# Kernel optimization log

Hardware: AMD Instinct MI355X
Metric: run time of the kernel (lower is better)

## Reference

```python
import jax, jax.numpy as jnp
import numpy as np

B, N, IN_DIM, HID, OUT, HEADS = 2, 1024, 64, 64, 64, 4
PHD1, PHD2 = HID // HEADS, OUT // HEADS
SLOPE = 0.2  # PyG GATv2Conv default negative_slope
EPS = 1e-12  # F.normalize eps


def _gatv2_dense(x, Wl, Wr, att, bias, heads, phd, mask):
    """Dense GATv2 layer over a full adjacency mask.
    x: [B,N,Din]; Wl/Wr: [Din, heads*phd]; att: [heads,phd]; bias: [heads*phd];
    mask: [N,N] bool, mask[i,j]=True means edge j->i exists.
    """
    Bb, Nn, _ = x.shape
    xl = (x @ Wl).reshape(Bb, Nn, heads, phd)  # source features
    xr = (x @ Wr).reshape(Bb, Nn, heads, phd)  # target features
    # s[b,i,j,h,p] = leaky_relu(xr[b,i] + xl[b,j])  (GATv2)
    s = jax.nn.leaky_relu(xr[:, :, None] + xl[:, None, :], SLOPE)
    e = jnp.einsum('bijhp,hp->bijh', s, att)  # [B,Ni,Nj,H]
    e = jnp.where(mask[None, :, :, None], e, -jnp.inf)
    alpha = jax.nn.softmax(e, axis=2)  # softmax over source nodes j
    out = jnp.einsum('bijh,bjhp->bihp', alpha, xl).reshape(Bb, Nn, heads * phd)
    return out + bias


def setup_inputs() -> dict:
    key = jax.random.key(0)
    ks = jax.random.split(key, 10)
    sc = 0.1
    return {
        'x': jax.random.normal(ks[0], (B, N, IN_DIM), jnp.float32),
        'embedding': jax.random.normal(ks[1], (N, HID), jnp.float32),
        'Wl1': jax.random.normal(ks[2], (IN_DIM, HEADS * PHD1), jnp.float32) * sc,
        'Wr1': jax.random.normal(ks[3], (IN_DIM, HEADS * PHD1), jnp.float32) * sc,
        'att1': jax.random.normal(ks[4], (HEADS, PHD1), jnp.float32) * sc,
        'b1': jnp.zeros((HEADS * PHD1,), jnp.float32),
        'Wl2': jax.random.normal(ks[5], (HID, HEADS * PHD2), jnp.float32) * sc,
        'Wr2': jax.random.normal(ks[6], (HID, HEADS * PHD2), jnp.float32) * sc,
        'att2': jax.random.normal(ks[7], (HEADS, PHD2), jnp.float32) * sc,
        'b2': jnp.zeros((HEADS * PHD2,), jnp.float32),
    }


def reference(x, embedding, Wl1, Wr1, att1, b1, Wl2, Wr2, att2, b2):
    # AdaptiveAdjacency: cosine-similarity adjacency; only its nonzero pattern is used.
    norm = jnp.maximum(jnp.linalg.norm(embedding, axis=1, keepdims=True), EPS)
    ne = embedding / norm
    adj = ne @ ne.T  # [N,N]
    # edge set = adj.nonzero(); GATv2Conv(add_self_loops=True) guarantees diagonal
    mask = (adj != 0) | jnp.eye(N, dtype=bool)
    h = jax.nn.relu(_gatv2_dense(x, Wl1, Wr1, att1, b1, HEADS, PHD1, mask))
    # dropout(0.3) in eval mode -> identity
    return _gatv2_dense(h, Wl2, Wr2, att2, b2, HEADS, PHD2, mask)
```

## Files before the change

### kernel.cpp

```cpp
#include <hip/hip_runtime.h>
#include <math.h>

#define NN 1024
#define BB 2
#define D 64
#define NHEAD 4
#define LOG2E 1.4426950408889634f
#define MST 65

template <int CTRL>
__device__ __forceinline__ float dpp_mov(float x) {
    int xi = __builtin_bit_cast(int, x);
    int r = __builtin_amdgcn_update_dpp(0, xi, CTRL, 0xF, 0xF, true);
    return __builtin_bit_cast(float, r);
}
template <int CTRL>
__device__ __forceinline__ unsigned dpp_movi(unsigned x) {
    int r = __builtin_amdgcn_update_dpp(0, (int)x, CTRL, 0xF, 0xF, true);
    return (unsigned)r;
}

__device__ __forceinline__ float dpp_rowsum16(float t) {
    t += dpp_mov<0x111>(t);
    t += dpp_mov<0x112>(t);
    t += dpp_mov<0x114>(t);
    t += dpp_mov<0x118>(t);
    return t;
}

__global__ __launch_bounds__(256) void k_mask_gemm(
    const float* __restrict__ emb, unsigned char* __restrict__ mask,
    const float* __restrict__ A, const float* __restrict__ Wl,
    const float* __restrict__ Wr, const float* __restrict__ att,
    float* __restrict__ xl, float* __restrict__ xr, float* __restrict__ alE)
{
    __shared__ float SH[64 * MST * 2];
    int tid = threadIdx.x;
    if (blockIdx.x < 256) {
        float* As = SH;
        float* Bs = SH + 64 * MST;
        int ib = (blockIdx.x & 15) << 6;
        int jb = (blockIdx.x >> 4) << 6;

        #pragma unroll
        for (int r = 0; r < 4; ++r) {
            int q = tid + (r << 8);
            int row = q >> 4, c4 = (q & 15) << 2;
            float4 a = *(const float4*)&emb[(ib + row) * D + c4];
            float4 b = *(const float4*)&emb[(jb + row) * D + c4];
            As[row * MST + c4 + 0] = a.x; As[row * MST + c4 + 1] = a.y;
            As[row * MST + c4 + 2] = a.z; As[row * MST + c4 + 3] = a.w;
            Bs[row * MST + c4 + 0] = b.x; Bs[row * MST + c4 + 1] = b.y;
            Bs[row * MST + c4 + 2] = b.z; Bs[row * MST + c4 + 3] = b.w;
        }
        __syncthreads();

        int i0 = (tid >> 4) << 2;
        int j0 = (tid & 15) << 2;
        float acc[4][4] = {};
        #pragma unroll 8
        for (int k = 0; k < 64; ++k) {
            float a0 = As[(i0 + 0) * MST + k];
            float a1 = As[(i0 + 1) * MST + k];
            float a2 = As[(i0 + 2) * MST + k];
            float a3 = As[(i0 + 3) * MST + k];
            float b0 = Bs[(j0 + 0) * MST + k];
            float b1 = Bs[(j0 + 1) * MST + k];
            float b2 = Bs[(j0 + 2) * MST + k];
            float b3 = Bs[(j0 + 3) * MST + k];
            acc[0][0] = fmaf(a0, b0, acc[0][0]); acc[0][1] = fmaf(a0, b1, acc[0][1]);
            acc[0][2] = fmaf(a0, b2, acc[0][2]); acc[0][3] = fmaf(a0, b3, acc[0][3]);
            acc[1][0] = fmaf(a1, b0, acc[1][0]); acc[1][1] = fmaf(a1, b1, acc[1][1]);
            acc[1][2] = fmaf(a1, b2, acc[1][2]); acc[1][3] = fmaf(a1, b3, acc[1][3]);
            acc[2][0] = fmaf(a2, b0, acc[2][0]); acc[2][1] = fmaf(a2, b1, acc[2][1]);
            acc[2][2] = fmaf(a2, b2, acc[2][2]); acc[2][3] = fmaf(a2, b3, acc[2][3]);
            acc[3][0] = fmaf(a3, b0, acc[3][0]); acc[3][1] = fmaf(a3, b1, acc[3][1]);
            acc[3][2] = fmaf(a3, b2, acc[3][2]); acc[3][3] = fmaf(a3, b3, acc[3][3]);
        }
        #pragma unroll
        for (int r = 0; r < 4; ++r) {
            int gi = ib + i0 + r;
            uchar4 m;
            m.x = (acc[r][0] != 0.f || gi == jb + j0 + 0) ? 1 : 0;
            m.y = (acc[r][1] != 0.f || gi == jb + j0 + 1) ? 1 : 0;
            m.z = (acc[r][2] != 0.f || gi == jb + j0 + 2) ? 1 : 0;
            m.w = (acc[r][3] != 0.f || gi == jb + j0 + 3) ? 1 : 0;
            *(uchar4*)&mask[gi * NN + jb + j0] = m;
        }
    } else {
        float* wl = SH;
        float* wr = SH + 4096;
        for (int t = tid; t < 4096; t += 256) { wl[t] = Wl[t]; wr[t] = Wr[t]; }
        __syncthreads();
        int r = (blockIdx.x - 256) * 4 + (tid >> 6);
        int c = tid & 63;
        float av = att[c];
        const float* arow = A + r * 64;
        float accl = 0.f, accr = 0.f;
        #pragma unroll
        for (int p = 0; p < 64; ++p) {
            float a = arow[p];
            accl = fmaf(a, wl[p * 64 + c], accl);
            accr = fmaf(a, wr[p * 64 + c], accr);
        }
        int cp = (((c >> 2) & 3) << 4) | ((c >> 4) << 2) | (c & 3);
        xl[r * 64 + cp] = accl;
        xr[r * 64 + c] = accr;
        float t = dpp_rowsum16(accl * av);
        if ((c & 15) == 15) alE[(r << 2) | (c >> 4)] = 0.6f * LOG2E * t;
    }
}

template <bool RELU, bool FUSEG>
__global__ __launch_bounds__(256, 2) void k_attn(
    const float* __restrict__ xlp, const float* __restrict__ xr,
    const float* __restrict__ att, const float* __restrict__ alE,
    const float* __restrict__ bias, const unsigned char* __restrict__ mask,
    float* __restrict__ out,
    const float* __restrict__ Wl2, const float* __restrict__ Wr2,
    const float* __restrict__ att2,
    float* __restrict__ xl2, float* __restrict__ xr2, float* __restrict__ alE2)
{
    __shared__ __align__(16) float XS[8192];
    __shared__ float Opart[4][4][4][64];
    __shared__ float Lpart[4][4][4][NHEAD];
    __shared__ float RES[4][64];

    int tid = threadIdx.x;
    int wave = tid >> 6, lane = tid & 63;
    int h = lane & 3, jl = lane >> 2;
    int b = blockIdx.x >> 8;
    int i0 = (blockIdx.x & 255) << 2;

    const float* xlb = xlp + (b << 16);

    float at[16], xr0f[16], xr1f[16], xr2f[16], xr3f[16];
    {
        const float* ap = att + (h << 4);
        const float* r0 = xr + (((b << 10) + i0) << 6) + (h << 4);
        const float* r1 = r0 + 64;
        const float* r2 = r0 + 128;
        const float* r3 = r0 + 192;
        #pragma unroll
        for (int c = 0; c < 4; ++c) {
            *(float4*)&at[c << 2]   = *(const float4*)(ap + (c << 2));
            *(float4*)&xr0f[c << 2] = *(const float4*)(r0 + (c << 2));
            *(float4*)&xr1f[c << 2] = *(const float4*)(r1 + (c << 2));
            *(float4*)&xr2f[c << 2] = *(const float4*)(r2 + (c << 2));
            *(float4*)&xr3f[c << 2] = *(const float4*)(r3 + (c << 2));
        }
        #pragma unroll
        for (int p = 0; p < 16; ++p) at[p] *= 0.4f * LOG2E;
    }
    float ar0, ar1, ar2, ar3;
    {
        float s0[4], s1[4], s2[4], s3[4];
        #pragma unroll
        for (int c = 0; c < 4; ++c) {
            float t0 = 0.f, t1 = 0.f, t2 = 0.f, t3 = 0.f;
            #pragma unroll
            for (int r = 0; r < 4; ++r) {
                int p = (c << 2) + r;
                float a = at[p];
                t0 = fmaf(a, xr0f[p], t0);
                t1 = fmaf(a, xr1f[p], t1);
                t2 = fmaf(a, xr2f[p], t2);
                t3 = fmaf(a, xr3f[p], t3);
            }
            s0[c] = t0; s1[c] = t1; s2[c] = t2; s3[c] = t3;
        }
        ar0 = 1.5f * ((s0[0] + s0[1]) + (s0[2] + s0[3]));
        ar1 = 1.5f * ((s1[0] + s1[1]) + (s1[2] + s1[3]));
        ar2 = 1.5f * ((s2[0] + s2[1]) + (s2[2] + s2[3]));
        ar3 = 1.5f * ((s3[0] + s3[1]) + (s3[2] + s3[3]));
    }

    unsigned mb0, mb1, mb2, mb3;
    {
        const unsigned char* mp = mask + i0 * NN + (wave << 8) + jl;
        int hh = h << 6;
        unsigned n0 = (unsigned)mp[hh] | ((unsigned)mp[hh + 16] << 1)
                    | ((unsigned)mp[hh + 32] << 2) | ((unsigned)mp[hh + 48] << 3);
        mp += NN;
        unsigned n1 = (unsigned)mp[hh] | ((unsigned)mp[hh + 16] << 1)
                    | ((unsigned)mp[hh + 32] << 2) | ((unsigned)mp[hh + 48] << 3);
        mp += NN;
        unsigned n2 = (unsigned)mp[hh] | ((unsigned)mp[hh + 16] << 1)
                    | ((unsigned)mp[hh + 32] << 2) | ((unsigned)mp[hh + 48] << 3);
        mp += NN;
        unsigned n3 = (unsigned)mp[hh] | ((unsigned)mp[hh + 16] << 1)
                    | ((unsigned)mp[hh + 32] << 2) | ((unsigned)mp[hh + 48] << 3);
        unsigned v0 = n0 << (h << 2), v1 = n1 << (h << 2);
        unsigned v2 = n2 << (h << 2), v3 = n3 << (h << 2);
        v0 |= dpp_movi<0xB1>(v0); v0 |= dpp_movi<0x4E>(v0);
        v1 |= dpp_movi<0xB1>(v1); v1 |= dpp_movi<0x4E>(v1);
        v2 |= dpp_movi<0xB1>(v2); v2 |= dpp_movi<0x4E>(v2);
        v3 |= dpp_movi<0xB1>(v3); v3 |= dpp_movi<0x4E>(v3);
        mb0 = v0; mb1 = v1; mb2 = v2; mb3 = v3;
    }

    float O0[16], O1[16], O2[16], O3[16];
    float lq0 = 0.f, lq1 = 0.f, lq2 = 0.f, lq3 = 0.f;
    #pragma unroll
    for (int p = 0; p < 16; ++p) { O0[p] = 0.f; O1[p] = 0.f; O2[p] = 0.f; O3[p] = 0.f; }

    const float* tb = xlb + (wave << 14);
    float* XB = XS + (wave << 11);
    int l4 = lane << 2;
    int rowoff = (lane >> 4) << 6;
    int sb = (lane & 15) ^ (lane >> 4);
    int A0 = rowoff + (sb << 2);
    int A1 = rowoff + ((sb ^ 4) << 2);
    int qx = (jl >> 2) & 1;
    int rb = (jl << 6) + ((h ^ (jl & 3)) << 2);
    const float* alp = alE + (b << 12) + (wave << 10) + lane;

    float4 gA0, gA1, gA2, gA3, gB0, gB1, gB2, gB3;
    {
        const float* p = tb + l4;
        gA0 = *(const float4*)p;         gA1 = *(const float4*)(p + 256);
        gA2 = *(const float4*)(p + 512); gA3 = *(const float4*)(p + 768);
        p = tb + 1024 + l4;
        gB0 = *(const float4*)p;         gB1 = *(const float4*)(p + 256);
        gB2 = *(const float4*)(p + 512); gB3 = *(const float4*)(p + 768);
        *(float4*)&XB[A0] = gA0;         *(float4*)&XB[256 + A1] = gA1;
        *(float4*)&XB[512 + A0] = gA2;   *(float4*)&XB[768 + A1] = gA3;
        p = tb + 2048 + l4;
        gA0 = *(const float4*)p;         gA1 = *(const float4*)(p + 256);
        gA2 = *(const float4*)(p + 512); gA3 = *(const float4*)(p + 768);
    }

    #pragma unroll 2
    for (int s = 0; s < 16; ++s) {
        if ((s & 1) == 0) {
            if (s < 15) {
                float* w = XB + (((s + 1) & 1) << 10);
                *(float4*)&w[A0] = gB0;         *(float4*)&w[256 + A1] = gB1;
                *(float4*)&w[512 + A0] = gB2;   *(float4*)&w[768 + A1] = gB3;
            }
            if (s < 13) {
                const float* p = tb + ((s + 3) << 10) + l4;
                gB0 = *(const float4*)p;         gB1 = *(const float4*)(p + 256);
                gB2 = *(const float4*)(p + 512); gB3 = *(const float4*)(p + 768);
            }
        } else {
            if (s < 15) {
                float* w = XB + (((s + 1) & 1) << 10);
                *(float4*)&w[A0] = gA0;         *(float4*)&w[256 + A1] = gA1;
                *(float4*)&w[512 + A0] = gA2;   *(float4*)&w[768 + A1] = gA3;
            }
            if (s < 13) {
                const float* p = tb + ((s + 3) << 10) + l4;
                gA0 = *(const float4*)p;         gA1 = *(const float4*)(p + 256);
                gA2 = *(const float4*)(p + 512); gA3 = *(const float4*)(p + 768);
            }
        }

        const float* XBr = XB + ((s & 1) << 10);
        float xv[16];
        *(float4*)&xv[0]  = *(const float4*)&XBr[rb + (((0 ^ qx)) << 4)];
        *(float4*)&xv[4]  = *(const float4*)&XBr[rb + (((1 ^ qx)) << 4)];
        *(float4*)&xv[8]  = *(const float4*)&XBr[rb + (((2 ^ qx)) << 4)];
        *(float4*)&xv[12] = *(const float4*)&XBr[rb + (((3 ^ qx)) << 4)];
        float alr = alp[s << 6];
        bool m0 = (mb0 >> s) & 1, m1 = (mb1 >> s) & 1;
        bool m2 = (mb2 >> s) & 1, m3 = (mb3 >> s) & 1;

        float s0[4], s1[4], s2[4], s3[4];
        #pragma unroll
        for (int c = 0; c < 4; ++c) {
            float t0 = 0.f, t1 = 0.f, t2 = 0.f, t3 = 0.f;
            #pragma unroll
            for (int r = 0; r < 4; ++r) {
                int p = (c << 2) + r;
                float a = at[p], xvv = xv[p];
                t0 = fmaf(a, __builtin_fabsf(xr0f[p] + xvv), t0);
                t1 = fmaf(a, __builtin_fabsf(xr1f[p] + xvv), t1);
                t2 = fmaf(a, __builtin_fabsf(xr2f[p] + xvv), t2);
                t3 = fmaf(a, __builtin_fabsf(xr3f[p] + xvv), t3);
            }
            s0[c] = t0; s1[c] = t1; s2[c] = t2; s3[c] = t3;
        }
        float e0 = ((s0[0] + s0[1]) + (s0[2] + s0[3])) + (ar0 + alr);
        float e1 = ((s1[0] + s1[1]) + (s1[2] + s1[3])) + (ar1 + alr);
        float e2 = ((s2[0] + s2[1]) + (s2[2] + s2[3])) + (ar2 + alr);
        float e3 = ((s3[0] + s3[1]) + (s3[2] + s3[3])) + (ar3 + alr);
        float pe0 = m0 ? __builtin_amdgcn_exp2f(e0) : 0.f;
        float pe1 = m1 ? __builtin_amdgcn_exp2f(e1) : 0.f;
        float pe2 = m2 ? __builtin_amdgcn_exp2f(e2) : 0.f;
        float pe3 = m3 ? __builtin_amdgcn_exp2f(e3) : 0.f;
        lq0 += pe0; lq1 += pe1; lq2 += pe2; lq3 += pe3;
        #pragma unroll
        for (int p = 0; p < 16; ++p) {
            float xvv = xv[p];
            O0[p] = fmaf(pe0, xvv, O0[p]);
            O1[p] = fmaf(pe1, xvv, O1[p]);
            O2[p] = fmaf(pe2, xvv, O2[p]);
            O3[p] = fmaf(pe3, xvv, O3[p]);
        }
    }

    if constexpr (FUSEG) {
        __syncthreads();
        for (int t = tid; t < 4096; t += 256) { XS[t] = Wl2[t]; XS[4096 + t] = Wr2[t]; }
    }

    #pragma unroll
    for (int p = 0; p < 16; ++p) {
        O0[p] += dpp_mov<0x114>(O0[p]);  O0[p] += dpp_mov<0x118>(O0[p]);
        O1[p] += dpp_mov<0x114>(O1[p]);  O1[p] += dpp_mov<0x118>(O1[p]);
        O2[p] += dpp_mov<0x114>(O2[p]);  O2[p] += dpp_mov<0x118>(O2[p]);
        O3[p] += dpp_mov<0x114>(O3[p]);  O3[p] += dpp_mov<0x118>(O3[p]);
    }
    lq0 += dpp_mov<0x114>(lq0);  lq0 += dpp_mov<0x118>(lq0);
    lq1 += dpp_mov<0x114>(lq1);  lq1 += dpp_mov<0x118>(lq1);
    lq2 += dpp_mov<0x114>(lq2);  lq2 += dpp_mov<0x118>(lq2);
    lq3 += dpp_mov<0x114>(lq3);  lq3 += dpp_mov<0x118>(lq3);

    if ((lane & 15) >= 12) {
        int k = lane >> 4;
        #pragma unroll
        for (int c = 0; c < 4; ++c) {
            *(float4*)&Opart[0][wave][k][(h << 4) + (c << 2)] = *(const float4*)&O0[c << 2];
            *(float4*)&Opart[1][wave][k][(h << 4) + (c << 2)] = *(const float4*)&O1[c << 2];
            *(float4*)&Opart[2][wave][k][(h << 4) + (c << 2)] = *(const float4*)&O2[c << 2];
            *(float4*)&Opart[3][wave][k][(h << 4) + (c << 2)] = *(const float4*)&O3[c << 2];
        }
        Lpart[0][wave][k][h] = lq0;
        Lpart[1][wave][k][h] = lq1;
        Lpart[2][wave][k][h] = lq2;
        Lpart[3][wave][k][h] = lq3;
    }
    __syncthreads();

    {
        int ii = tid >> 6, c = tid & 63;
        float o = 0.f, l = 0.f;
        #pragma unroll
        for (int w = 0; w < 4; ++w)
            #pragma unroll
            for (int k = 0; k < 4; ++k) {
                o += Opart[ii][w][k][c];
                l += Lpart[ii][w][k][c >> 4];
            }
        float res = o / l + bias[c];
        if (RELU) res = fmaxf(res, 0.f);
        if constexpr (FUSEG) {
            RES[ii][c] = res;
        } else {
            out[((b << 10) + i0 + ii) * D + c] = res;
        }
    }

    if constexpr (FUSEG) {
        __syncthreads();
        int ii = tid >> 6, c = tid & 63;
        int rr = (blockIdx.x << 2) + ii;
        float av = att2[c];
        const float* arow = &RES[ii][0];
        float accl = 0.f, accr = 0.f;
        #pragma unroll
        for (int p = 0; p < 64; ++p) {
            float a = arow[p];
            accl = fmaf(a, XS[p * 64 + c], accl);
            accr = fmaf(a, XS[4096 + p * 64 + c], accr);
        }
        int cp = (((c >> 2) & 3) << 4) | ((c >> 4) << 2) | (c & 3);
        xl2[rr * 64 + cp] = accl;
        xr2[rr * 64 + c] = accr;
        float t = dpp_rowsum16(accl * av);
        if ((c & 15) == 15) alE2[(rr << 2) | (c >> 4)] = 0.6f * LOG2E * t;
    }
}

extern "C" void kernel_launch(void* const* d_in, const int* in_sizes, int n_in,
                              void* d_out, int out_size, void* d_ws, size_t ws_size,
                              hipStream_t stream) {
    const float* x    = (const float*)d_in[0];
    const float* emb  = (const float*)d_in[1];
    const float* Wl1  = (const float*)d_in[2];
    const float* Wr1  = (const float*)d_in[3];
    const float* att1 = (const float*)d_in[4];
    const float* b1   = (const float*)d_in[5];
    const float* Wl2  = (const float*)d_in[6];
    const float* Wr2  = (const float*)d_in[7];
    const float* att2 = (const float*)d_in[8];
    const float* b2   = (const float*)d_in[9];
    float* out = (float*)d_out;

    unsigned char* mask = (unsigned char*)d_ws;
    float* xl   = (float*)(mask + NN * NN);
    float* xr   = xl + BB * NN * D;
    float* xl2  = xr + BB * NN * D;
    float* alE  = xl2 + BB * NN * D;
    float* xr2  = alE + BB * NN * NHEAD;
    float* alE2 = xr2 + BB * NN * D;

    k_mask_gemm<<<256 + BB * NN / 4, 256, 0, stream>>>(emb, mask, x, Wl1, Wr1, att1, xl, xr, alE);

    k_attn<true, true><<<BB * NN / 4, 256, 0, stream>>>(
        xl, xr, att1, alE, b1, mask, xl2 ,
        Wl2, Wr2, att2, xl2, xr2, alE2);

    k_attn<false, false><<<BB * NN / 4, 256, 0, stream>>>(
        xl2, xr2, att2, alE2, b2, mask, out,
        Wl2, Wr2, att2, xl2, xr2, alE2 );
}
```

Baseline: 122.0 us.

## Process eight target rows per attention block instead of four

Each attention block now handles 8 target nodes instead of 4, so every source-feature tile staged in shared memory is reused across twice as many rows, halving global xl traffic per output. Grid size is halved to 256 blocks and launch bounds drop to one block per CU to fit the doubled register accumulators. This trades occupancy and parallelism (only 256 blocks on a 256-CU part) for reuse, and raises register pressure with risk of spills.

```diff
diff --git a/kernel.cpp b/kernel.cpp
--- a/kernel.cpp
+++ b/kernel.cpp
@@ -112,7 +112,7 @@
 }
 
 template <bool RELU, bool FUSEG>
-__global__ __launch_bounds__(256, 2) void k_attn(
+__global__ __launch_bounds__(256, 1) void k_attn(
     const float* __restrict__ xlp, const float* __restrict__ xr,
     const float* __restrict__ att, const float* __restrict__ alE,
     const float* __restrict__ bias, const unsigned char* __restrict__ mask,
@@ -122,42 +122,46 @@
     float* __restrict__ xl2, float* __restrict__ xr2, float* __restrict__ alE2)
 {
     __shared__ __align__(16) float XS[8192];
-    __shared__ float Opart[4][4][4][64];
-    __shared__ float Lpart[4][4][4][NHEAD];
-    __shared__ float RES[4][64];
+    __shared__ float Opart[8][4][4][64];
+    __shared__ float Lpart[8][4][4][NHEAD];
+    __shared__ float RES[8][64];
 
     int tid = threadIdx.x;
     int wave = tid >> 6, lane = tid & 63;
     int h = lane & 3, jl = lane >> 2;
-    int b = blockIdx.x >> 8;
-    int i0 = (blockIdx.x & 255) << 2;
+    int b = blockIdx.x >> 7;
+    int i0 = (blockIdx.x & 127) << 3;
 
     const float* xlb = xlp + (b << 16);
 
-    float at[16], xr0f[16], xr1f[16], xr2f[16], xr3f[16];
+    float at[16];
+    float xr0f[16], xr1f[16], xr2f[16], xr3f[16];
+    float xr4f[16], xr5f[16], xr6f[16], xr7f[16];
     {
         const float* ap = att + (h << 4);
         const float* r0 = xr + (((b << 10) + i0) << 6) + (h << 4);
-        const float* r1 = r0 + 64;
-        const float* r2 = r0 + 128;
-        const float* r3 = r0 + 192;
         #pragma unroll
         for (int c = 0; c < 4; ++c) {
             *(float4*)&at[c << 2]   = *(const float4*)(ap + (c << 2));
             *(float4*)&xr0f[c << 2] = *(const float4*)(r0 + (c << 2));
-            *(float4*)&xr1f[c << 2] = *(const float4*)(r1 + (c << 2));
-            *(float4*)&xr2f[c << 2] = *(const float4*)(r2 + (c << 2));
-            *(float4*)&xr3f[c << 2] = *(const float4*)(r3 + (c << 2));
+            *(float4*)&xr1f[c << 2] = *(const float4*)(r0 + 64 + (c << 2));
+            *(float4*)&xr2f[c << 2] = *(const float4*)(r0 + 128 + (c << 2));
+            *(float4*)&xr3f[c << 2] = *(const float4*)(r0 + 192 + (c << 2));
+            *(float4*)&xr4f[c << 2] = *(const float4*)(r0 + 256 + (c << 2));
+            *(float4*)&xr5f[c << 2] = *(const float4*)(r0 + 320 + (c << 2));
+            *(float4*)&xr6f[c << 2] = *(const float4*)(r0 + 384 + (c << 2));
+            *(float4*)&xr7f[c << 2] = *(const float4*)(r0 + 448 + (c << 2));
         }
         #pragma unroll
         for (int p = 0; p < 16; ++p) at[p] *= 0.4f * LOG2E;
     }
-    float ar0, ar1, ar2, ar3;
+    float ar0, ar1, ar2, ar3, ar4, ar5, ar6, ar7;
     {
-        float s0[4], s1[4], s2[4], s3[4];
+        float s0[4], s1[4], s2[4], s3[4], s4[4], s5[4], s6[4], s7[4];
         #pragma unroll
         for (int c = 0; c < 4; ++c) {
             float t0 = 0.f, t1 = 0.f, t2 = 0.f, t3 = 0.f;
+            float t4 = 0.f, t5 = 0.f, t6 = 0.f, t7 = 0.f;
             #pragma unroll
             for (int r = 0; r < 4; ++r) {
                 int p = (c << 2) + r;
@@ -166,43 +170,58 @@
                 t1 = fmaf(a, xr1f[p], t1);
                 t2 = fmaf(a, xr2f[p], t2);
                 t3 = fmaf(a, xr3f[p], t3);
+                t4 = fmaf(a, xr4f[p], t4);
+                t5 = fmaf(a, xr5f[p], t5);
+                t6 = fmaf(a, xr6f[p], t6);
+                t7 = fmaf(a, xr7f[p], t7);
             }
             s0[c] = t0; s1[c] = t1; s2[c] = t2; s3[c] = t3;
+            s4[c] = t4; s5[c] = t5; s6[c] = t6; s7[c] = t7;
         }
         ar0 = 1.5f * ((s0[0] + s0[1]) + (s0[2] + s0[3]));
         ar1 = 1.5f * ((s1[0] + s1[1]) + (s1[2] + s1[3]));
         ar2 = 1.5f * ((s2[0] + s2[1]) + (s2[2] + s2[3]));
         ar3 = 1.5f * ((s3[0] + s3[1]) + (s3[2] + s3[3]));
-    }
-
-    unsigned mb0, mb1, mb2, mb3;
+        ar4 = 1.5f * ((s4[0] + s4[1]) + (s4[2] + s4[3]));
+        ar5 = 1.5f * ((s5[0] + s5[1]) + (s5[2] + s5[3]));
+        ar6 = 1.5f * ((s6[0] + s6[1]) + (s6[2] + s6[3]));
+        ar7 = 1.5f * ((s7[0] + s7[1]) + (s7[2] + s7[3]));
+    }
+
+    unsigned mb0, mb1, mb2, mb3, mb4, mb5, mb6, mb7;
     {
         const unsigned char* mp = mask + i0 * NN + (wave << 8) + jl;
         int hh = h << 6;
-        unsigned n0 = (unsigned)mp[hh] | ((unsigned)mp[hh + 16] << 1)
-                    | ((unsigned)mp[hh + 32] << 2) | ((unsigned)mp[hh + 48] << 3);
-        mp += NN;
-        unsigned n1 = (unsigned)mp[hh] | ((unsigned)mp[hh + 16] << 1)
-                    | ((unsigned)mp[hh + 32] << 2) | ((unsigned)mp[hh + 48] << 3);
-        mp += NN;
-        unsigned n2 = (unsigned)mp[hh] | ((unsigned)mp[hh + 16] << 1)
-                    | ((unsigned)mp[hh + 32] << 2) | ((unsigned)mp[hh + 48] << 3);
-        mp += NN;
-        unsigned n3 = (unsigned)mp[hh] | ((unsigned)mp[hh + 16] << 1)
-                    | ((unsigned)mp[hh + 32] << 2) | ((unsigned)mp[hh + 48] << 3);
-        unsigned v0 = n0 << (h << 2), v1 = n1 << (h << 2);
-        unsigned v2 = n2 << (h << 2), v3 = n3 << (h << 2);
+        unsigned nv[8];
+        #pragma unroll
+        for (int rw = 0; rw < 8; ++rw) {
+            nv[rw] = (unsigned)mp[hh] | ((unsigned)mp[hh + 16] << 1)
+                   | ((unsigned)mp[hh + 32] << 2) | ((unsigned)mp[hh + 48] << 3);
+            mp += NN;
+        }
+        unsigned sh = h << 2;
+        unsigned v0 = nv[0] << sh, v1 = nv[1] << sh, v2 = nv[2] << sh, v3 = nv[3] << sh;
+        unsigned v4 = nv[4] << sh, v5 = nv[5] << sh, v6 = nv[6] << sh, v7 = nv[7] << sh;
         v0 |= dpp_movi<0xB1>(v0); v0 |= dpp_movi<0x4E>(v0);
         v1 |= dpp_movi<0xB1>(v1); v1 |= dpp_movi<0x4E>(v1);
         v2 |= dpp_movi<0xB1>(v2); v2 |= dpp_movi<0x4E>(v2);
         v3 |= dpp_movi<0xB1>(v3); v3 |= dpp_movi<0x4E>(v3);
+        v4 |= dpp_movi<0xB1>(v4); v4 |= dpp_movi<0x4E>(v4);
+        v5 |= dpp_movi<0xB1>(v5); v5 |= dpp_movi<0x4E>(v5);
+        v6 |= dpp_movi<0xB1>(v6); v6 |= dpp_movi<0x4E>(v6);
+        v7 |= dpp_movi<0xB1>(v7); v7 |= dpp_movi<0x4E>(v7);
         mb0 = v0; mb1 = v1; mb2 = v2; mb3 = v3;
-    }
-
-    float O0[16], O1[16], O2[16], O3[16];
+        mb4 = v4; mb5 = v5; mb6 = v6; mb7 = v7;
+    }
+
+    float O0[16], O1[16], O2[16], O3[16], O4[16], O5[16], O6[16], O7[16];
     float lq0 = 0.f, lq1 = 0.f, lq2 = 0.f, lq3 = 0.f;
+    float lq4 = 0.f, lq5 = 0.f, lq6 = 0.f, lq7 = 0.f;
     #pragma unroll
-    for (int p = 0; p < 16; ++p) { O0[p] = 0.f; O1[p] = 0.f; O2[p] = 0.f; O3[p] = 0.f; }
+    for (int p = 0; p < 16; ++p) {
+        O0[p] = 0.f; O1[p] = 0.f; O2[p] = 0.f; O3[p] = 0.f;
+        O4[p] = 0.f; O5[p] = 0.f; O6[p] = 0.f; O7[p] = 0.f;
+    }
 
     const float* tb = xlb + (wave << 14);
     float* XB = XS + (wave << 11);
@@ -265,11 +284,14 @@
         float alr = alp[s << 6];
         bool m0 = (mb0 >> s) & 1, m1 = (mb1 >> s) & 1;
         bool m2 = (mb2 >> s) & 1, m3 = (mb3 >> s) & 1;
-
-        float s0[4], s1[4], s2[4], s3[4];
+        bool m4 = (mb4 >> s) & 1, m5 = (mb5 >> s) & 1;
+        bool m6 = (mb6 >> s) & 1, m7 = (mb7 >> s) & 1;
+
+        float s0[4], s1[4], s2[4], s3[4], s4[4], s5[4], s6[4], s7[4];
         #pragma unroll
         for (int c = 0; c < 4; ++c) {
             float t0 = 0.f, t1 = 0.f, t2 = 0.f, t3 = 0.f;
+            float t4 = 0.f, t5 = 0.f, t6 = 0.f, t7 = 0.f;
             #pragma unroll
             for (int r = 0; r < 4; ++r) {
                 int p = (c << 2) + r;
@@ -278,18 +300,32 @@
                 t1 = fmaf(a, __builtin_fabsf(xr1f[p] + xvv), t1);
                 t2 = fmaf(a, __builtin_fabsf(xr2f[p] + xvv), t2);
                 t3 = fmaf(a, __builtin_fabsf(xr3f[p] + xvv), t3);
+                t4 = fmaf(a, __builtin_fabsf(xr4f[p] + xvv), t4);
+                t5 = fmaf(a, __builtin_fabsf(xr5f[p] + xvv), t5);
+                t6 = fmaf(a, __builtin_fabsf(xr6f[p] + xvv), t6);
+                t7 = fmaf(a, __builtin_fabsf(xr7f[p] + xvv), t7);
             }
             s0[c] = t0; s1[c] = t1; s2[c] = t2; s3[c] = t3;
+            s4[c] = t4; s5[c] = t5; s6[c] = t6; s7[c] = t7;
         }
         float e0 = ((s0[0] + s0[1]) + (s0[2] + s0[3])) + (ar0 + alr);
         float e1 = ((s1[0] + s1[1]) + (s1[2] + s1[3])) + (ar1 + alr);
         float e2 = ((s2[0] + s2[1]) + (s2[2] + s2[3])) + (ar2 + alr);
         float e3 = ((s3[0] + s3[1]) + (s3[2] + s3[3])) + (ar3 + alr);
+        float e4 = ((s4[0] + s4[1]) + (s4[2] + s4[3])) + (ar4 + alr);
+        float e5 = ((s5[0] + s5[1]) + (s5[2] + s5[3])) + (ar5 + alr);
+        float e6 = ((s6[0] + s6[1]) + (s6[2] + s6[3])) + (ar6 + alr);
+        float e7 = ((s7[0] + s7[1]) + (s7[2] + s7[3])) + (ar7 + alr);
         float pe0 = m0 ? __builtin_amdgcn_exp2f(e0) : 0.f;
         float pe1 = m1 ? __builtin_amdgcn_exp2f(e1) : 0.f;
         float pe2 = m2 ? __builtin_amdgcn_exp2f(e2) : 0.f;
         float pe3 = m3 ? __builtin_amdgcn_exp2f(e3) : 0.f;
+        float pe4 = m4 ? __builtin_amdgcn_exp2f(e4) : 0.f;
+        float pe5 = m5 ? __builtin_amdgcn_exp2f(e5) : 0.f;
+        float pe6 = m6 ? __builtin_amdgcn_exp2f(e6) : 0.f;
+        float pe7 = m7 ? __builtin_amdgcn_exp2f(e7) : 0.f;
         lq0 += pe0; lq1 += pe1; lq2 += pe2; lq3 += pe3;
+        lq4 += pe4; lq5 += pe5; lq6 += pe6; lq7 += pe7;
         #pragma unroll
         for (int p = 0; p < 16; ++p) {
             float xvv = xv[p];
@@ -297,6 +333,10 @@
             O1[p] = fmaf(pe1, xvv, O1[p]);
             O2[p] = fmaf(pe2, xvv, O2[p]);
             O3[p] = fmaf(pe3, xvv, O3[p]);
+            O4[p] = fmaf(pe4, xvv, O4[p]);
+            O5[p] = fmaf(pe5, xvv, O5[p]);
+            O6[p] = fmaf(pe6, xvv, O6[p]);
+            O7[p] = fmaf(pe7, xvv, O7[p]);
         }
     }
 
@@ -311,11 +351,19 @@
         O1[p] += dpp_mov<0x114>(O1[p]);  O1[p] += dpp_mov<0x118>(O1[p]);
         O2[p] += dpp_mov<0x114>(O2[p]);  O2[p] += dpp_mov<0x118>(O2[p]);
         O3[p] += dpp_mov<0x114>(O3[p]);  O3[p] += dpp_mov<0x118>(O3[p]);
+        O4[p] += dpp_mov<0x114>(O4[p]);  O4[p] += dpp_mov<0x118>(O4[p]);
+        O5[p] += dpp_mov<0x114>(O5[p]);  O5[p] += dpp_mov<0x118>(O5[p]);
+        O6[p] += dpp_mov<0x114>(O6[p]);  O6[p] += dpp_mov<0x118>(O6[p]);
+        O7[p] += dpp_mov<0x114>(O7[p]);  O7[p] += dpp_mov<0x118>(O7[p]);
     }
     lq0 += dpp_mov<0x114>(lq0);  lq0 += dpp_mov<0x118>(lq0);
     lq1 += dpp_mov<0x114>(lq1);  lq1 += dpp_mov<0x118>(lq1);
     lq2 += dpp_mov<0x114>(lq2);  lq2 += dpp_mov<0x118>(lq2);
     lq3 += dpp_mov<0x114>(lq3);  lq3 += dpp_mov<0x118>(lq3);
+    lq4 += dpp_mov<0x114>(lq4);  lq4 += dpp_mov<0x118>(lq4);
+    lq5 += dpp_mov<0x114>(lq5);  lq5 += dpp_mov<0x118>(lq5);
+    lq6 += dpp_mov<0x114>(lq6);  lq6 += dpp_mov<0x118>(lq6);
+    lq7 += dpp_mov<0x114>(lq7);  lq7 += dpp_mov<0x118>(lq7);
 
     if ((lane & 15) >= 12) {
         int k = lane >> 4;
@@ -325,51 +373,67 @@
             *(float4*)&Opart[1][wave][k][(h << 4) + (c << 2)] = *(const float4*)&O1[c << 2];
             *(float4*)&Opart[2][wave][k][(h << 4) + (c << 2)] = *(const float4*)&O2[c << 2];
             *(float4*)&Opart[3][wave][k][(h << 4) + (c << 2)] = *(const float4*)&O3[c << 2];
+            *(float4*)&Opart[4][wave][k][(h << 4) + (c << 2)] = *(const float4*)&O4[c << 2];
+            *(float4*)&Opart[5][wave][k][(h << 4) + (c << 2)] = *(const float4*)&O5[c << 2];
+            *(float4*)&Opart[6][wave][k][(h << 4) + (c << 2)] = *(const float4*)&O6[c << 2];
+            *(float4*)&Opart[7][wave][k][(h << 4) + (c << 2)] = *(const float4*)&O7[c << 2];
         }
         Lpart[0][wave][k][h] = lq0;
         Lpart[1][wave][k][h] = lq1;
         Lpart[2][wave][k][h] = lq2;
         Lpart[3][wave][k][h] = lq3;
+        Lpart[4][wave][k][h] = lq4;
+        Lpart[5][wave][k][h] = lq5;
+        Lpart[6][wave][k][h] = lq6;
+        Lpart[7][wave][k][h] = lq7;
     }
     __syncthreads();
 
     {
-        int ii = tid >> 6, c = tid & 63;
-        float o = 0.f, l = 0.f;
-        #pragma unroll
-        for (int w = 0; w < 4; ++w)
+        int c = tid & 63;
+        #pragma unroll
+        for (int pass = 0; pass < 2; ++pass) {
+            int ii = (tid >> 6) + (pass << 2);
+            float o = 0.f, l = 0.f;
             #pragma unroll
-            for (int k = 0; k < 4; ++k) {
-                o += Opart[ii][w][k][c];
-                l += Lpart[ii][w][k][c >> 4];
-            }
-        float res = o / l + bias[c];
-        if (RELU) res = fmaxf(res, 0.f);
-        if constexpr (FUSEG) {
-            RES[ii][c] = res;
-        } else {
-            out[((b << 10) + i0 + ii) * D + c] = res;
+            for (int w = 0; w < 4; ++w)
+                #pragma unroll
+                for (int k = 0; k < 4; ++k) {
+                    o += Opart[ii][w][k][c];
+                    l += Lpart[ii][w][k][c >> 4];
+                }
+            float res = o / l + bias[c];
+            if (RELU) res = fmaxf(res, 0.f);
+            if constexpr (FUSEG) {
+                RES[ii][c] = res;
+            } else {
+                out[((b << 10) + i0 + ii) * D + c] = res;
+            }
         }
     }
 
     if constexpr (FUSEG) {
         __syncthreads();
-        int ii = tid >> 6, c = tid & 63;
-        int rr = (blockIdx.x << 2) + ii;
+        int c = tid & 63;
         float av = att2[c];
-        const float* arow = &RES[ii][0];
-        float accl = 0.f, accr = 0.f;
-        #pragma unroll
-        for (int p = 0; p < 64; ++p) {
-            float a = arow[p];
-            accl = fmaf(a, XS[p * 64 + c], accl);
-            accr = fmaf(a, XS[4096 + p * 64 + c], accr);
-        }
         int cp = (((c >> 2) & 3) << 4) | ((c >> 4) << 2) | (c & 3);
-        xl2[rr * 64 + cp] = accl;
-        xr2[rr * 64 + c] = accr;
-        float t = dpp_rowsum16(accl * av);
-        if ((c & 15) == 15) alE2[(rr << 2) | (c >> 4)] = 0.6f * LOG2E * t;
+        #pragma unroll
+        for (int pass = 0; pass < 2; ++pass) {
+            int ii = (tid >> 6) + (pass << 2);
+            int rr = (blockIdx.x << 3) + ii;
+            const float* arow = &RES[ii][0];
+            float accl = 0.f, accr = 0.f;
+            #pragma unroll
+            for (int p = 0; p < 64; ++p) {
+                float a = arow[p];
+                accl = fmaf(a, XS[p * 64 + c], accl);
+                accr = fmaf(a, XS[4096 + p * 64 + c], accr);
+            }
+            xl2[rr * 64 + cp] = accl;
+            xr2[rr * 64 + c] = accr;
+            float t = dpp_rowsum16(accl * av);
+            if ((c & 15) == 15) alE2[(rr << 2) | (c >> 4)] = 0.6f * LOG2E * t;
+        }
     }
 }
 
@@ -398,11 +462,11 @@
 
     k_mask_gemm<<<256 + BB * NN / 4, 256, 0, stream>>>(emb, mask, x, Wl1, Wr1, att1, xl, xr, alE);
 
-    k_attn<true, true><<<BB * NN / 4, 256, 0, stream>>>(
+    k_attn<true, true><<<BB * NN / 8, 256, 0, stream>>>(
         xl, xr, att1, alE, b1, mask, xl2 ,
         Wl2, Wr2, att2, xl2, xr2, alE2);
 
-    k_attn<false, false><<<BB * NN / 4, 256, 0, stream>>>(
+    k_attn<false, false><<<BB * NN / 8, 256, 0, stream>>>(
         xl2, xr2, att2, alE2, b2, mask, out,
         Wl2, Wr2, att2, xl2, xr2, alE2 );
 }
```

Result: slower. 173.8 us (+42.4%).
